# Optimization experiments

Hardware: AMD Instinct MI355X
Metric: run time of the kernel (lower is better)

## Reference

```python
import jax, jax.numpy as jnp
import numpy as np

# Static multi-scale pyramid configuration (matches src_spatial_shapes / level_start_index inputs)
LEVEL_SHAPES = [(128, 128), (64, 64), (32, 32), (16, 16)]  # (H, W) per level
NH, NL, NP = 8, 4, 4  # n_heads, n_levels, n_points
D = 256


def setup_inputs() -> dict:
    key = jax.random.key(0)
    ks = jax.random.split(key, 24)
    N, Lq = 4, 8192
    Lin = sum(h * w for h, w in LEVEL_SHAPES)  # 21760
    d_ff = 4 * D
    inp = {
        "tgt": jax.random.normal(ks[0], (N, Lq, D), jnp.float32),
        "query_pos": jax.random.normal(ks[1], (N, Lq, D), jnp.float32),
        "reference_points": jax.random.uniform(ks[2], (N, Lq, NL, 2), jnp.float32),
        "src": jax.random.normal(ks[3], (N, Lin, D), jnp.float32),
        "src_spatial_shapes": jnp.array(LEVEL_SHAPES, dtype=jnp.int64),
        "level_start_index": jnp.array(np.cumsum([0] + [h * w for h, w in LEVEL_SHAPES[:-1]]), dtype=jnp.int64),
        "src_padding_mask": jnp.zeros((N, Lin), dtype=bool),
        # MSDeformAttn params
        "W_off": jax.random.normal(ks[4], (D, NH * NL * NP * 2), jnp.float32) * 0.01,
        "b_off": jax.random.normal(ks[5], (NH * NL * NP * 2,), jnp.float32) * 0.01,
        "W_attn": jax.random.normal(ks[6], (D, NH * NL * NP), jnp.float32) * 0.02,
        "b_attn": jnp.zeros((NH * NL * NP,), jnp.float32),
        "W_val": jax.random.normal(ks[7], (D, D), jnp.float32) * 0.02,
        "b_val": jnp.zeros((D,), jnp.float32),
        "W_out": jax.random.normal(ks[8], (D, D), jnp.float32) * 0.02,
        "b_out": jnp.zeros((D,), jnp.float32),
        # LN + MLP params
        "ln1_g": jnp.ones((D,), jnp.float32),
        "ln1_b": jnp.zeros((D,), jnp.float32),
        "W_fc1": jax.random.normal(ks[9], (D, d_ff), jnp.float32) * 0.02,
        "b_fc1": jnp.zeros((d_ff,), jnp.float32),
        "W_fc2": jax.random.normal(ks[10], (d_ff, D), jnp.float32) * 0.02,
        "b_fc2": jnp.zeros((D,), jnp.float32),
        "ln2_g": jnp.ones((D,), jnp.float32),
        "ln2_b": jnp.zeros((D,), jnp.float32),
    }
    return inp


def _layer_norm(x, g, b, eps=1e-5):
    x32 = x.astype(jnp.float32)
    m = x32.mean(-1, keepdims=True)
    v = x32.var(-1, keepdims=True)
    return (((x32 - m) * jax.lax.rsqrt(v + eps)) * g + b).astype(x.dtype)


def _sample_level(value_flat, H, W, loc):
    # value_flat: [N, H*W, NH, hd]; loc: [N, Lq, NH, NP, 2] in [0,1]
    # torch.grid_sample align_corners=False, padding_mode='zeros'
    x = loc[..., 0] * W - 0.5
    y = loc[..., 1] * H - 0.5
    x0 = jnp.floor(x)
    y0 = jnp.floor(y)
    dx, dy = x - x0, y - y0
    N, Lq, nh, P = x.shape
    hd = value_flat.shape[-1]
    corners = [
        (x0, y0, (1.0 - dx) * (1.0 - dy)),
        (x0 + 1.0, y0, dx * (1.0 - dy)),
        (x0, y0 + 1.0, (1.0 - dx) * dy),
        (x0 + 1.0, y0 + 1.0, dx * dy),
    ]
    out = jnp.zeros((N, Lq * P, nh, hd), value_flat.dtype)
    for cx, cy, w in corners:
        valid = (cx >= 0) & (cx <= W - 1) & (cy >= 0) & (cy <= H - 1)
        ix = jnp.clip(cx, 0, W - 1).astype(jnp.int32)
        iy = jnp.clip(cy, 0, H - 1).astype(jnp.int32)
        idx = (iy * W + ix).transpose(0, 1, 3, 2).reshape(N, Lq * P, nh)[..., None]
        v = jnp.take_along_axis(value_flat, idx, axis=1)  # [N, Lq*P, NH, hd]
        ww = (w * valid).transpose(0, 1, 3, 2).reshape(N, Lq * P, nh)[..., None]
        out = out + v * ww
    return out.reshape(N, Lq, P, nh, hd)  # [N, Lq, NP, NH, hd]


def reference(tgt, query_pos, reference_points, src, src_spatial_shapes,
              level_start_index, src_padding_mask,
              W_off, b_off, W_attn, b_attn, W_val, b_val, W_out, b_out,
              ln1_g, ln1_b, W_fc1, b_fc1, W_fc2, b_fc2, ln2_g, ln2_b):
    N, Lq, _ = tgt.shape
    hd = D // NH
    q = tgt + query_pos

    # value projection + padding mask
    value = src @ W_val + b_val
    value = jnp.where(src_padding_mask[..., None], 0.0, value)
    value = value.reshape(N, -1, NH, hd)

    # sampling offsets and attention weights
    off = (q @ W_off + b_off).reshape(N, Lq, NH, NL, NP, 2)
    aw = (q @ W_attn + b_attn).reshape(N, Lq, NH, NL * NP)
    aw = jax.nn.softmax(aw, axis=-1).reshape(N, Lq, NH, NL, NP)

    # normalize offsets by (W, H) per level
    normalizer = jnp.array([[w, h] for (h, w) in LEVEL_SHAPES], jnp.float32)  # [NL, 2]
    loc = reference_points[:, :, None, :, None, :] + off / normalizer[None, None, None, :, None, :]

    out = jnp.zeros((N, Lq, NH, hd), value.dtype)
    start = 0
    for l, (H, W) in enumerate(LEVEL_SHAPES):
        vflat = value[:, start:start + H * W]
        start += H * W
        sampled = _sample_level(vflat, H, W, loc[:, :, :, l])  # [N, Lq, NP, NH, hd]
        w_l = aw[:, :, :, l].transpose(0, 1, 3, 2)[..., None]  # [N, Lq, NP, NH, 1]
        out = out + (sampled * w_l).sum(axis=2)
    attn_out = out.reshape(N, Lq, D) @ W_out + b_out

    # residual + LN + MLP (named 'gelu' but is ReLU in source) + LN
    x = _layer_norm(tgt + attn_out, ln1_g, ln1_b)
    h = jax.nn.relu(x @ W_fc1 + b_fc1) @ W_fc2 + b_fc2
    x = _layer_norm(x + h, ln2_g, ln2_b)
    return x
```

## Files before the change

### kernel.cpp

```cpp
#include <hip/hip_runtime.h>
#include <hip/hip_bf16.h>

constexpr int NB    = 4;
constexpr int LQ    = 8192;
constexpr int DM    = 256;
constexpr int NHEAD = 8;
constexpr int HD    = 32;
constexpr int LIN   = 21760;
constexpr int DFF   = 1024;
constexpr int MQ    = NB * LQ;
constexpr int MV    = NB * LIN;

typedef __attribute__((ext_vector_type(8))) short short8;
typedef __attribute__((ext_vector_type(4))) float f32x4;

__device__ __forceinline__ ushort f2b(float f) {
  union { __hip_bfloat16 h; ushort u; } c;
  c.h = __float2bfloat16(f);
  return c.u;
}
__device__ __forceinline__ float b2f(ushort u) {
  return __uint_as_float((unsigned int)u << 16);
}

__device__ __forceinline__ void load_lds16(const ushort* g, ushort* l) {
  __builtin_amdgcn_global_load_lds(
      (const __attribute__((address_space(1))) void*)g,
      (__attribute__((address_space(3))) void*)l, 16, 0, 0);
}

__global__ __launch_bounds__(256) void k_packw(const float* __restrict__ W,
                                               ushort* __restrict__ P,
                                               int K, int Nsrc, int n_base) {
  __shared__ float T[32][33];
  const int k0 = blockIdx.x * 32, n0 = blockIdx.y * 32;
  const int t = threadIdx.x;
  {
    const int r = t >> 3, c4 = t & 7;
    const float4 v = *reinterpret_cast<const float4*>(
        &W[(size_t)(k0 + r) * Nsrc + n0 + c4 * 4]);
    T[r][c4 * 4 + 0] = v.x;
    T[r][c4 * 4 + 1] = v.y;
    T[r][c4 * 4 + 2] = v.z;
    T[r][c4 * 4 + 3] = v.w;
  }
  __syncthreads();
  const int dn = t >> 3, q = t & 7;
  const int n = n_base + n0 + dn;
  const int k = k0 + q * 4;
  const int Tt = n >> 4, fr = n & 15, kg = (k >> 3) & 3;
  const int idx = Tt * (K >> 5) + (k >> 5);
  ushort4 o;
  o.x = f2b(T[q * 4 + 0][dn]);
  o.y = f2b(T[q * 4 + 1][dn]);
  o.z = f2b(T[q * 4 + 2][dn]);
  o.w = f2b(T[q * 4 + 3][dn]);
  *reinterpret_cast<ushort4*>(&P[(size_t)idx * 512 + (kg * 16 + fr) * 8 + (k & 7)]) = o;
}

template<int MODE, int ASRC>
__global__ __launch_bounds__(256) void k_gemm(
    const void* __restrict__ Ap, const float* __restrict__ A2,
    const ushort* __restrict__ BP,
    const float* __restrict__ bias, const float* __restrict__ bias2,
    void* __restrict__ out0, void* __restrict__ out1,
    int M, int N, int K) {
  __shared__ __align__(16) ushort SMEM[17408];
  ushort* As = SMEM;
  const int m0 = blockIdx.x * 128, n0 = blockIdx.y * 128;
  const int t = threadIdx.x, w = t >> 6, l = t & 63;
  const int wr = (w >> 1) * 64, wc = (w & 1) * 64;
  const int fr = l & 15, kg = l >> 4;
  const int lrow = l >> 3;
  const int sg = (l & 7) ^ lrow;
  const int Kg = K >> 5;

  f32x4 acc[4][4];
#pragma unroll
  for (int i = 0; i < 4; ++i)
#pragma unroll
    for (int j = 0; j < 4; ++j) acc[i][j] = f32x4{0.f, 0.f, 0.f, 0.f};

  const float* Af = (const float*)Ap;

  for (int k0 = 0; k0 < K; k0 += 64) {
    float4 fa[4][2];
#pragma unroll
    for (int i = 0; i < 4; ++i) {
      const float* ap = Af + (size_t)(m0 + i * 32 + w * 8 + lrow) * K + k0 + sg * 8;
      fa[i][0] = *reinterpret_cast<const float4*>(ap);
      fa[i][1] = *reinterpret_cast<const float4*>(ap + 4);
      if constexpr (ASRC == 2) {
        const float* ap2 = A2 + (size_t)(m0 + i * 32 + w * 8 + lrow) * K + k0 + sg * 8;
        const float4 x = *reinterpret_cast<const float4*>(ap2);
        const float4 y = *reinterpret_cast<const float4*>(ap2 + 4);
        fa[i][0].x += x.x; fa[i][0].y += x.y; fa[i][0].z += x.z; fa[i][0].w += x.w;
        fa[i][1].x += y.x; fa[i][1].y += y.y; fa[i][1].z += y.z; fa[i][1].w += y.w;
      }
    }
    __syncthreads();
#pragma unroll
    for (int i = 0; i < 4; ++i) {
      uint4 u;
      u.x = (unsigned int)f2b(fa[i][0].x) | ((unsigned int)f2b(fa[i][0].y) << 16);
      u.y = (unsigned int)f2b(fa[i][0].z) | ((unsigned int)f2b(fa[i][0].w) << 16);
      u.z = (unsigned int)f2b(fa[i][1].x) | ((unsigned int)f2b(fa[i][1].y) << 16);
      u.w = (unsigned int)f2b(fa[i][1].z) | ((unsigned int)f2b(fa[i][1].w) << 16);
      *reinterpret_cast<uint4*>(As + i * 2048 + w * 512 + l * 8) = u;
    }
    __syncthreads();
#pragma unroll
    for (int kk = 0; kk < 2; ++kk) {
      short8 a[4], b[4];
#pragma unroll
      for (int i = 0; i < 4; ++i)
        a[i] = *reinterpret_cast<const short8*>(
            &As[(wr + i * 16 + fr) * 64 + ((kk * 4 + kg) ^ (fr & 7)) * 8]);
#pragma unroll
      for (int i = 0; i < 4; ++i)
        b[i] = *reinterpret_cast<const short8*>(
            BP + ((size_t)((n0 >> 4) + (w & 1) * 4 + i) * Kg + (k0 >> 5) + kk) * 512 + l * 8);
#pragma unroll
      for (int mi = 0; mi < 4; ++mi)
#pragma unroll
        for (int ni = 0; ni < 4; ++ni)
          acc[mi][ni] = __builtin_amdgcn_mfma_f32_16x16x32_bf16(
              b[ni], a[mi], acc[mi][ni], 0, 0, 0);
    }
  }

  if constexpr (MODE == 0) {
    ushort (*LC)[136] = (ushort(*)[136])SMEM;
    __syncthreads();
#pragma unroll
    for (int ni = 0; ni < 4; ++ni) {
      const float4 bv = *reinterpret_cast<const float4*>(&bias[n0 + wc + ni * 16 + kg * 4]);
#pragma unroll
      for (int mi = 0; mi < 4; ++mi) {
        ushort4 p;
        p.x = f2b(acc[mi][ni][0] + bv.x);
        p.y = f2b(acc[mi][ni][1] + bv.y);
        p.z = f2b(acc[mi][ni][2] + bv.z);
        p.w = f2b(acc[mi][ni][3] + bv.w);
        *reinterpret_cast<ushort4*>(&LC[wr + mi * 16 + fr][wc + ni * 16 + kg * 4]) = p;
      }
    }
    __syncthreads();
    const int c = t & 15, rb = t >> 4;
#pragma unroll
    for (int i = 0; i < 8; ++i) {
      const int r = rb + i * 16;
      const uint4 vv = *reinterpret_cast<const uint4*>(&LC[r][c * 8]);
      *reinterpret_cast<uint4*>((ushort*)out0 + (size_t)(m0 + r) * N + n0 + c * 8) = vv;
    }
  } else {
    float (*LF)[132] = (float(*)[132])SMEM;
    const float* bp = (n0 < 256) ? bias + n0 : bias2;
    float* op = (n0 < 256) ? (float*)out0 + n0 : (float*)out1;
    const int ostride = (n0 < 256) ? 256 : 128;
#pragma unroll
    for (int p = 0; p < 2; ++p) {
      __syncthreads();
      if ((w >> 1) == p) {
#pragma unroll
        for (int ni = 0; ni < 4; ++ni) {
          const float4 bv = *reinterpret_cast<const float4*>(&bp[wc + ni * 16 + kg * 4]);
#pragma unroll
          for (int mi = 0; mi < 4; ++mi) {
            float4 v;
            v.x = acc[mi][ni][0] + bv.x; v.y = acc[mi][ni][1] + bv.y;
            v.z = acc[mi][ni][2] + bv.z; v.w = acc[mi][ni][3] + bv.w;
            *reinterpret_cast<float4*>(&LF[mi * 16 + fr][wc + ni * 16 + kg * 4]) = v;
          }
        }
      }
      __syncthreads();
      const int c = t & 31, rb = t >> 5;
#pragma unroll
      for (int i = 0; i < 8; ++i) {
        const int r = rb + i * 8;
        const float4 vv = *reinterpret_cast<const float4*>(&LF[r][c * 4]);
        *reinterpret_cast<float4*>(&op[(size_t)(m0 + p * 64 + r) * ostride + c * 4]) = vv;
      }
    }
  }
}

__global__ __launch_bounds__(256) void k_outln(
    const ushort* __restrict__ A, const ushort* __restrict__ BP,
    const float* __restrict__ bias, const float* __restrict__ res,
    const float* __restrict__ g, const float* __restrict__ bvec,
    ushort* __restrict__ out, int K) {
  __shared__ __align__(16) ushort SMEM[17408];
  ushort* As = SMEM;
  const int m0 = blockIdx.x * 64;
  const int t = threadIdx.x, w = t >> 6, l = t & 63;
  const int wc = w * 64;
  const int fr = l & 15, kg = l >> 4;
  const int lrow = l >> 3;
  const int sg = (l & 7) ^ lrow;
  const int Kg = K >> 5;

  f32x4 acc[4][4];
#pragma unroll
  for (int i = 0; i < 4; ++i)
#pragma unroll
    for (int j = 0; j < 4; ++j) acc[i][j] = f32x4{0.f, 0.f, 0.f, 0.f};

  for (int k0 = 0; k0 < K; k0 += 64) {
    __syncthreads();
#pragma unroll
    for (int i = 0; i < 2; ++i)
      load_lds16(A + (size_t)(m0 + i * 32 + w * 8 + lrow) * K + k0 + sg * 8,
                 As + i * 2048 + w * 512);
    __syncthreads();
#pragma unroll
    for (int kk = 0; kk < 2; ++kk) {
      short8 a[4], b[4];
#pragma unroll
      for (int i = 0; i < 4; ++i)
        a[i] = *reinterpret_cast<const short8*>(
            &As[(i * 16 + fr) * 64 + ((kk * 4 + kg) ^ (fr & 7)) * 8]);
#pragma unroll
      for (int i = 0; i < 4; ++i)
        b[i] = *reinterpret_cast<const short8*>(
            BP + ((size_t)(w * 4 + i) * Kg + (k0 >> 5) + kk) * 512 + l * 8);
#pragma unroll
      for (int mi = 0; mi < 4; ++mi)
#pragma unroll
        for (int ni = 0; ni < 4; ++ni)
          acc[mi][ni] = __builtin_amdgcn_mfma_f32_16x16x32_bf16(
              b[ni], a[mi], acc[mi][ni], 0, 0, 0);
    }
  }

  ushort (*LY)[272] = (ushort(*)[272])SMEM;
  __syncthreads();
#pragma unroll
  for (int ni = 0; ni < 4; ++ni) {
    const float4 bv = *reinterpret_cast<const float4*>(&bias[wc + ni * 16 + kg * 4]);
#pragma unroll
    for (int mi = 0; mi < 4; ++mi) {
      ushort4 p;
      p.x = f2b(acc[mi][ni][0] + bv.x);
      p.y = f2b(acc[mi][ni][1] + bv.y);
      p.z = f2b(acc[mi][ni][2] + bv.z);
      p.w = f2b(acc[mi][ni][3] + bv.w);
      *reinterpret_cast<ushort4*>(&LY[mi * 16 + fr][wc + ni * 16 + kg * 4]) = p;
    }
  }
  __syncthreads();

  const int c = t & 31, rb = t >> 5;
#pragma unroll
  for (int i = 0; i < 8; ++i) {
    const int r = rb + i * 8;
    const uint4 yy = *reinterpret_cast<const uint4*>(&LY[r][c * 8]);
    const unsigned int yw[4] = {yy.x, yy.y, yy.z, yy.w};
    float v[8];
#pragma unroll
    for (int j = 0; j < 4; ++j) {
      v[2 * j]     = __uint_as_float(yw[j] << 16);
      v[2 * j + 1] = __uint_as_float(yw[j] & 0xffff0000u);
    }
    const float* rp = res + (size_t)(m0 + r) * 256 + c * 8;
    const float4 r0 = *reinterpret_cast<const float4*>(rp);
    const float4 r1 = *reinterpret_cast<const float4*>(rp + 4);
    v[0] += r0.x; v[1] += r0.y; v[2] += r0.z; v[3] += r0.w;
    v[4] += r1.x; v[5] += r1.y; v[6] += r1.z; v[7] += r1.w;
    float s = 0.f, ss = 0.f;
#pragma unroll
    for (int j = 0; j < 8; ++j) { s += v[j]; ss += v[j] * v[j]; }
#pragma unroll
    for (int o = 1; o < 32; o <<= 1) {
      s  += __shfl_xor(s, o);
      ss += __shfl_xor(ss, o);
    }
    const float m = s * (1.f / 256.f);
    const float inv = rsqrtf(ss * (1.f / 256.f) - m * m + 1e-5f);
    const float4 g0 = *reinterpret_cast<const float4*>(&g[c * 8]);
    const float4 g1 = *reinterpret_cast<const float4*>(&g[c * 8 + 4]);
    const float4 b0 = *reinterpret_cast<const float4*>(&bvec[c * 8]);
    const float4 b1 = *reinterpret_cast<const float4*>(&bvec[c * 8 + 4]);
    uint4 u;
    u.x = (unsigned int)f2b((v[0] - m) * inv * g0.x + b0.x) |
          ((unsigned int)f2b((v[1] - m) * inv * g0.y + b0.y) << 16);
    u.y = (unsigned int)f2b((v[2] - m) * inv * g0.z + b0.z) |
          ((unsigned int)f2b((v[3] - m) * inv * g0.w + b0.w) << 16);
    u.z = (unsigned int)f2b((v[4] - m) * inv * g1.x + b1.x) |
          ((unsigned int)f2b((v[5] - m) * inv * g1.y + b1.y) << 16);
    u.w = (unsigned int)f2b((v[6] - m) * inv * g1.z + b1.z) |
          ((unsigned int)f2b((v[7] - m) * inv * g1.w + b1.w) << 16);
    *reinterpret_cast<uint4*>(out + (size_t)(m0 + r) * 256 + c * 8) = u;
  }
}

__global__ __launch_bounds__(256) void k_ffn(
    const ushort* __restrict__ X, const ushort* __restrict__ W1P,
    const float* __restrict__ bb1, const ushort* __restrict__ W2P,
    const float* __restrict__ bb2, const float* __restrict__ g2,
    const float* __restrict__ b2v, float* __restrict__ out) {
  __shared__ __align__(16) ushort SMEM[24576];
  ushort* Xs = SMEM;
  ushort* Hs = SMEM + 16384;
  const int m0 = blockIdx.x * 64;
  const int t = threadIdx.x, w = t >> 6, l = t & 63;
  const int fr = l & 15, kg = l >> 4;

#pragma unroll
  for (int i = 0; i < 8; ++i) {
    const int gi = w * 8 + i;
    const int row = gi * 2 + (l >> 5);
    load_lds16(X + (size_t)(m0 + row) * 256 + (((l & 31) ^ (row & 7)) * 8),
               Xs + gi * 512);
  }
  __syncthreads();

  f32x4 acc2[4][4];
#pragma unroll
  for (int i = 0; i < 4; ++i)
#pragma unroll
    for (int j = 0; j < 4; ++j) acc2[i][j] = f32x4{0.f, 0.f, 0.f, 0.f};

  for (int c = 0; c < 8; ++c) {
    f32x4 acc1[4][2];
#pragma unroll
    for (int i = 0; i < 4; ++i)
#pragma unroll
      for (int j = 0; j < 2; ++j) acc1[i][j] = f32x4{0.f, 0.f, 0.f, 0.f};
#pragma unroll
    for (int ks = 0; ks < 8; ++ks) {
      short8 a[4], b[2];
#pragma unroll
      for (int mi = 0; mi < 4; ++mi)
        a[mi] = *reinterpret_cast<const short8*>(
            &Xs[(mi * 16 + fr) * 256 + ((ks * 4 + kg) ^ (fr & 7)) * 8]);
#pragma unroll
      for (int ni = 0; ni < 2; ++ni)
        b[ni] = *reinterpret_cast<const short8*>(
            W1P + ((size_t)(c * 8 + w * 2 + ni) * 8 + ks) * 512 + l * 8);
#pragma unroll
      for (int mi = 0; mi < 4; ++mi)
#pragma unroll
        for (int ni = 0; ni < 2; ++ni)
          acc1[mi][ni] = __builtin_amdgcn_mfma_f32_16x16x32_bf16(
              b[ni], a[mi], acc1[mi][ni], 0, 0, 0);
    }
    __syncthreads();
#pragma unroll
    for (int ni = 0; ni < 2; ++ni) {
      const float4 bv = *reinterpret_cast<const float4*>(
          &bb1[c * 128 + w * 32 + ni * 16 + kg * 4]);
#pragma unroll
      for (int mi = 0; mi < 4; ++mi) {
        const int row = mi * 16 + fr;
        const int gcol = w * 4 + ni * 2 + (kg >> 1);
        ushort4 p;
        p.x = f2b(fmaxf(acc1[mi][ni][0] + bv.x, 0.f));
        p.y = f2b(fmaxf(acc1[mi][ni][1] + bv.y, 0.f));
        p.z = f2b(fmaxf(acc1[mi][ni][2] + bv.z, 0.f));
        p.w = f2b(fmaxf(acc1[mi][ni][3] + bv.w, 0.f));
        *reinterpret_cast<ushort4*>(
            &Hs[row * 128 + ((gcol ^ (fr & 7)) * 8) + (kg & 1) * 4]) = p;
      }
    }
    __syncthreads();
#pragma unroll
    for (int ks2 = 0; ks2 < 4; ++ks2) {
      short8 a2[4], b2[4];
#pragma unroll
      for (int mi = 0; mi < 4; ++mi)
        a2[mi] = *reinterpret_cast<const short8*>(
            &Hs[(mi * 16 + fr) * 128 + ((ks2 * 4 + kg) ^ (fr & 7)) * 8]);
#pragma unroll
      for (int ni = 0; ni < 4; ++ni)
        b2[ni] = *reinterpret_cast<const short8*>(
            W2P + ((size_t)(w * 4 + ni) * 32 + c * 4 + ks2) * 512 + l * 8);
#pragma unroll
      for (int mi = 0; mi < 4; ++mi)
#pragma unroll
        for (int ni = 0; ni < 4; ++ni)
          acc2[mi][ni] = __builtin_amdgcn_mfma_f32_16x16x32_bf16(
              b2[ni], a2[mi], acc2[mi][ni], 0, 0, 0);
    }
  }

#pragma unroll
  for (int ni = 0; ni < 4; ++ni) {
    const int colb = w * 64 + ni * 16 + kg * 4;
    const float4 bv = *reinterpret_cast<const float4*>(&bb2[colb]);
    const int g = w * 8 + ni * 2 + (kg >> 1);
#pragma unroll
    for (int mi = 0; mi < 4; ++mi) {
      const int row = mi * 16 + fr;
      const ushort4 xr = *reinterpret_cast<const ushort4*>(
          &Xs[row * 256 + ((g ^ (fr & 7)) * 8) + (kg & 1) * 4]);
      acc2[mi][ni][0] += bv.x + b2f(xr.x);
      acc2[mi][ni][1] += bv.y + b2f(xr.y);
      acc2[mi][ni][2] += bv.z + b2f(xr.z);
      acc2[mi][ni][3] += bv.w + b2f(xr.w);
    }
  }
  __syncthreads();

  ushort (*LY)[272] = (ushort(*)[272])SMEM;
#pragma unroll
  for (int ni = 0; ni < 4; ++ni) {
#pragma unroll
    for (int mi = 0; mi < 4; ++mi) {
      ushort4 p;
      p.x = f2b(acc2[mi][ni][0]);
      p.y = f2b(acc2[mi][ni][1]);
      p.z = f2b(acc2[mi][ni][2]);
      p.w = f2b(acc2[mi][ni][3]);
      *reinterpret_cast<ushort4*>(&LY[mi * 16 + fr][w * 64 + ni * 16 + kg * 4]) = p;
    }
  }
  __syncthreads();

  const int cc = t & 31, rb = t >> 5;
#pragma unroll
  for (int i = 0; i < 8; ++i) {
    const int r = rb + i * 8;
    const uint4 yy = *reinterpret_cast<const uint4*>(&LY[r][cc * 8]);
    const unsigned int yw[4] = {yy.x, yy.y, yy.z, yy.w};
    float v[8];
#pragma unroll
    for (int j = 0; j < 4; ++j) {
      v[2 * j]     = __uint_as_float(yw[j] << 16);
      v[2 * j + 1] = __uint_as_float(yw[j] & 0xffff0000u);
    }
    float s = 0.f, ss = 0.f;
#pragma unroll
    for (int j = 0; j < 8; ++j) { s += v[j]; ss += v[j] * v[j]; }
#pragma unroll
    for (int o = 1; o < 32; o <<= 1) {
      s  += __shfl_xor(s, o);
      ss += __shfl_xor(ss, o);
    }
    const float m = s * (1.f / 256.f);
    const float inv = rsqrtf(ss * (1.f / 256.f) - m * m + 1e-5f);
    const float4 g0 = *reinterpret_cast<const float4*>(&g2[cc * 8]);
    const float4 g1 = *reinterpret_cast<const float4*>(&g2[cc * 8 + 4]);
    const float4 b0 = *reinterpret_cast<const float4*>(&b2v[cc * 8]);
    const float4 b1 = *reinterpret_cast<const float4*>(&b2v[cc * 8 + 4]);
    float* opp = out + (size_t)(m0 + r) * 256 + cc * 8;
    float4 q0, q1;
    q0.x = (v[0] - m) * inv * g0.x + b0.x;
    q0.y = (v[1] - m) * inv * g0.y + b0.y;
    q0.z = (v[2] - m) * inv * g0.z + b0.z;
    q0.w = (v[3] - m) * inv * g0.w + b0.w;
    q1.x = (v[4] - m) * inv * g1.x + b1.x;
    q1.y = (v[5] - m) * inv * g1.y + b1.y;
    q1.z = (v[6] - m) * inv * g1.z + b1.z;
    q1.w = (v[7] - m) * inv * g1.w + b1.w;
    *reinterpret_cast<float4*>(opp) = q0;
    *reinterpret_cast<float4*>(opp + 4) = q1;
  }
}

__global__ __launch_bounds__(256) void k_softmax(const float* __restrict__ logits,
                                                 float* __restrict__ aw) {
  const int g = blockIdx.x * 256 + threadIdx.x;
  const float* p = logits + (size_t)g * 16;
  float mx = p[0];
#pragma unroll
  for (int i = 1; i < 16; ++i) mx = fmaxf(mx, p[i]);
  float e[16], s = 0.f;
#pragma unroll
  for (int i = 0; i < 16; ++i) { e[i] = __expf(p[i] - mx); s += e[i]; }
  const float inv = 1.f / s;
  float* o = aw + (size_t)g * 16;
#pragma unroll
  for (int i = 0; i < 16; ++i) o[i] = e[i] * inv;
}

__global__ __launch_bounds__(256) void k_sample(
    const float* __restrict__ refp, const float* __restrict__ off_ws,
    const float* __restrict__ aw_ws, const ushort* __restrict__ value,
    ushort* __restrict__ pre) {
  const int tid = blockIdx.x * 256 + threadIdx.x;
  const int cg = tid & 3;
  const int h  = (tid >> 2) & 7;
  const int nq = tid >> 5;
  const int n  = nq >> 13;

  const float* rp = refp + (size_t)nq * 8;
  const float* op = off_ws + (size_t)nq * DM + h * 32;
  const float* ap = aw_ws + (size_t)nq * 128 + h * 16;
  const ushort* vb = value + (size_t)n * LIN * DM + h * HD + cg * 8;

  float acc[8];
#pragma unroll
  for (int j = 0; j < 8; ++j) acc[j] = 0.f;

  const int WL[4] = {128, 64, 32, 16};
  const int ST[4] = {0, 16384, 20480, 21504};

#pragma unroll
  for (int lvl = 0; lvl < 4; ++lvl) {
    const int Wl = WL[lvl];
    const float fW = (float)Wl;
    const float invW = 1.f / fW;
    const float rx = rp[lvl * 2 + 0];
    const float ry = rp[lvl * 2 + 1];
    const ushort* vl = vb + (size_t)ST[lvl] * DM;
#pragma unroll
    for (int p = 0; p < 4; ++p) {
      const float xx = (rx + op[(lvl * 4 + p) * 2 + 0] * invW) * fW - 0.5f;
      const float yy = (ry + op[(lvl * 4 + p) * 2 + 1] * invW) * fW - 0.5f;
      const float a = ap[lvl * 4 + p];
      const float x0 = floorf(xx), y0 = floorf(yy);
      const float dx = xx - x0, dy = yy - y0;
      const bool vx0 = (x0 >= 0.f) && (x0 <= fW - 1.f);
      const bool vx1 = (x0 + 1.f >= 0.f) && (x0 + 1.f <= fW - 1.f);
      const bool vy0 = (y0 >= 0.f) && (y0 <= fW - 1.f);
      const bool vy1 = (y0 + 1.f >= 0.f) && (y0 + 1.f <= fW - 1.f);
      const int ix0 = min(max((int)x0, 0), Wl - 1);
      const int ix1 = min(max((int)x0 + 1, 0), Wl - 1);
      const int iy0 = min(max((int)y0, 0), Wl - 1);
      const int iy1 = min(max((int)y0 + 1, 0), Wl - 1);
      const float w00 = (vx0 && vy0) ? (1.f - dx) * (1.f - dy) * a : 0.f;
      const float w10 = (vx1 && vy0) ? dx * (1.f - dy) * a : 0.f;
      const float w01 = (vx0 && vy1) ? (1.f - dx) * dy * a : 0.f;
      const float w11 = (vx1 && vy1) ? dx * dy * a : 0.f;
      const ushort* r0 = vl + (size_t)iy0 * Wl * DM;
      const ushort* r1 = vl + (size_t)iy1 * Wl * DM;
      const uint4 u00 = *reinterpret_cast<const uint4*>(r0 + ix0 * DM);
      const uint4 u10 = *reinterpret_cast<const uint4*>(r0 + ix1 * DM);
      const uint4 u01 = *reinterpret_cast<const uint4*>(r1 + ix0 * DM);
      const uint4 u11 = *reinterpret_cast<const uint4*>(r1 + ix1 * DM);
      const unsigned int uu00[4] = {u00.x, u00.y, u00.z, u00.w};
      const unsigned int uu10[4] = {u10.x, u10.y, u10.z, u10.w};
      const unsigned int uu01[4] = {u01.x, u01.y, u01.z, u01.w};
      const unsigned int uu11[4] = {u11.x, u11.y, u11.z, u11.w};
#pragma unroll
      for (int i = 0; i < 4; ++i) {
        acc[2 * i]     += __uint_as_float(uu00[i] << 16) * w00;
        acc[2 * i + 1] += __uint_as_float(uu00[i] & 0xffff0000u) * w00;
        acc[2 * i]     += __uint_as_float(uu10[i] << 16) * w10;
        acc[2 * i + 1] += __uint_as_float(uu10[i] & 0xffff0000u) * w10;
        acc[2 * i]     += __uint_as_float(uu01[i] << 16) * w01;
        acc[2 * i + 1] += __uint_as_float(uu01[i] & 0xffff0000u) * w01;
        acc[2 * i]     += __uint_as_float(uu11[i] << 16) * w11;
        acc[2 * i + 1] += __uint_as_float(uu11[i] & 0xffff0000u) * w11;
      }
    }
  }

  uint4 o;
  o.x = (unsigned int)f2b(acc[0]) | ((unsigned int)f2b(acc[1]) << 16);
  o.y = (unsigned int)f2b(acc[2]) | ((unsigned int)f2b(acc[3]) << 16);
  o.z = (unsigned int)f2b(acc[4]) | ((unsigned int)f2b(acc[5]) << 16);
  o.w = (unsigned int)f2b(acc[6]) | ((unsigned int)f2b(acc[7]) << 16);
  *reinterpret_cast<uint4*>(pre + (size_t)nq * DM + h * HD + cg * 8) = o;
}

extern "C" void kernel_launch(void* const* d_in, const int* in_sizes, int n_in,
                              void* d_out, int out_size, void* d_ws, size_t ws_size,
                              hipStream_t stream) {
  const float* tgt   = (const float*)d_in[0];
  const float* qpos  = (const float*)d_in[1];
  const float* refp  = (const float*)d_in[2];
  const float* src   = (const float*)d_in[3];
  const float* Woff  = (const float*)d_in[7];
  const float* boff  = (const float*)d_in[8];
  const float* Wattn = (const float*)d_in[9];
  const float* battn = (const float*)d_in[10];
  const float* Wval  = (const float*)d_in[11];
  const float* bval  = (const float*)d_in[12];
  const float* Wout  = (const float*)d_in[13];
  const float* bout  = (const float*)d_in[14];
  const float* g1    = (const float*)d_in[15];
  const float* b1    = (const float*)d_in[16];
  const float* W1    = (const float*)d_in[17];
  const float* bb1   = (const float*)d_in[18];
  const float* W2    = (const float*)d_in[19];
  const float* bb2   = (const float*)d_in[20];
  const float* g2    = (const float*)d_in[21];
  const float* b2v   = (const float*)d_in[22];
  float* out = (float*)d_out;

  char* ws = (char*)d_ws;
  float*  offb   = (float*)(ws + 0);
  ushort* valueb = (ushort*)(ws + 44564480);
  ushort* preb   = (ushort*)(ws + 89128960);
  float*  logits = (float*)(ws + 105906176);
  float*  awb    = (float*)(ws + 122683392);
  ushort* xb     = (ushort*)(ws + 0);
  ushort* wvalP  = (ushort*)(ws + 156237824);
  ushort* wqP    = wvalP + 65536;
  ushort* woutP  = wqP + 98304;
  ushort* w1P    = woutP + 65536;
  ushort* w2P    = w1P + 262144;

  hipLaunchKernelGGL(k_packw, dim3(8, 8), dim3(256), 0, stream, Wval, wvalP, 256, 256, 0);
  hipLaunchKernelGGL(k_packw, dim3(8, 8), dim3(256), 0, stream, Woff, wqP, 256, 256, 0);
  hipLaunchKernelGGL(k_packw, dim3(8, 4), dim3(256), 0, stream, Wattn, wqP, 256, 128, 256);
  hipLaunchKernelGGL(k_packw, dim3(8, 8), dim3(256), 0, stream, Wout, woutP, 256, 256, 0);
  hipLaunchKernelGGL(k_packw, dim3(8, 32), dim3(256), 0, stream, W1, w1P, 256, 1024, 0);
  hipLaunchKernelGGL(k_packw, dim3(32, 8), dim3(256), 0, stream, W2, w2P, 1024, 256, 0);

  hipLaunchKernelGGL((k_gemm<0, 1>), dim3(MV / 128, 2), dim3(256), 0, stream,
                     (const void*)src, (const float*)nullptr, wvalP, bval,
                     (const float*)nullptr, (void*)valueb, (void*)nullptr,
                     MV, DM, DM);

  hipLaunchKernelGGL((k_gemm<3, 2>), dim3(MQ / 128, 3), dim3(256), 0, stream,
                     (const void*)tgt, qpos, wqP, boff, battn,
                     (void*)offb, (void*)logits, MQ, 384, DM);

  hipLaunchKernelGGL(k_softmax, dim3(MQ * 8 / 256), dim3(256), 0, stream, logits, awb);

  hipLaunchKernelGGL(k_sample, dim3(MQ * NHEAD * 4 / 256), dim3(256), 0, stream,
                     refp, offb, awb, valueb, preb);

  hipLaunchKernelGGL(k_outln, dim3(MQ / 64), dim3(256), 0, stream,
                     preb, woutP, bout, tgt, g1, b1, xb, DM);

  hipLaunchKernelGGL(k_ffn, dim3(MQ / 64), dim3(256), 0, stream,
                     xb, w1P, bb1, w2P, bb2, g2, b2v, out);
}
```

Measured before the change: 260.9 us.

## Fuse softmax into logit GEMM, store offsets as bf16, merge weight packing

Splits the query projection into a bf16 offset GEMM and a separate logit GEMM whose epilogue computes the per-head softmax, which removes the standalone softmax kernel and its fp32 logits round trip. The sampling offsets are now written and read as bf16, which halves that traffic but lowers offset precision. The sampler gains vectorized loads and a swizzled block order for cache locality, and the six weight-pack launches become one kernel. The tgt+qpos input is now read twice, once by each of the two query GEMMs.

```diff
diff --git a/kernel.cpp b/kernel.cpp
--- a/kernel.cpp
+++ b/kernel.cpp
@@ -29,11 +29,25 @@
       (__attribute__((address_space(3))) void*)l, 16, 0, 0);
 }
 
-__global__ __launch_bounds__(256) void k_packw(const float* __restrict__ W,
-                                               ushort* __restrict__ P,
-                                               int K, int Nsrc, int n_base) {
+__global__ __launch_bounds__(256) void k_packall(
+    const float* __restrict__ Wval, const float* __restrict__ Woff,
+    const float* __restrict__ Wattn, const float* __restrict__ Wout,
+    const float* __restrict__ W1, const float* __restrict__ W2,
+    ushort* __restrict__ wvalP, ushort* __restrict__ wqP,
+    ushort* __restrict__ woutP, ushort* __restrict__ w1P,
+    ushort* __restrict__ w2P) {
+  const int bid = blockIdx.x;
+  const float* W; ushort* P; int K, Nsrc, n_base, local;
+  if (bid < 64)       { W = Wval;  P = wvalP; K = 256;  Nsrc = 256;  n_base = 0;   local = bid; }
+  else if (bid < 128) { W = Woff;  P = wqP;   K = 256;  Nsrc = 256;  n_base = 0;   local = bid - 64; }
+  else if (bid < 160) { W = Wattn; P = wqP;   K = 256;  Nsrc = 128;  n_base = 256; local = bid - 128; }
+  else if (bid < 224) { W = Wout;  P = woutP; K = 256;  Nsrc = 256;  n_base = 0;   local = bid - 160; }
+  else if (bid < 480) { W = W1;    P = w1P;   K = 256;  Nsrc = 1024; n_base = 0;   local = bid - 224; }
+  else                { W = W2;    P = w2P;   K = 1024; Nsrc = 256;  n_base = 0;   local = bid - 480; }
+  const int kb = local % (K >> 5), nb = local / (K >> 5);
+  const int k0 = kb * 32, n0 = nb * 32;
+
   __shared__ float T[32][33];
-  const int k0 = blockIdx.x * 32, n0 = blockIdx.y * 32;
   const int t = threadIdx.x;
   {
     const int r = t >> 3, c4 = t & 7;
@@ -62,9 +76,8 @@
 __global__ __launch_bounds__(256) void k_gemm(
     const void* __restrict__ Ap, const float* __restrict__ A2,
     const ushort* __restrict__ BP,
-    const float* __restrict__ bias, const float* __restrict__ bias2,
-    void* __restrict__ out0, void* __restrict__ out1,
-    int M, int N, int K) {
+    const float* __restrict__ bias,
+    void* __restrict__ out0, int M, int N, int K) {
   __shared__ __align__(16) ushort SMEM[17408];
   ushort* As = SMEM;
   const int m0 = blockIdx.x * 128, n0 = blockIdx.y * 128;
@@ -129,59 +142,143 @@
     }
   }
 
-  if constexpr (MODE == 0) {
-    ushort (*LC)[136] = (ushort(*)[136])SMEM;
-    __syncthreads();
-#pragma unroll
-    for (int ni = 0; ni < 4; ++ni) {
-      const float4 bv = *reinterpret_cast<const float4*>(&bias[n0 + wc + ni * 16 + kg * 4]);
-#pragma unroll
-      for (int mi = 0; mi < 4; ++mi) {
-        ushort4 p;
-        p.x = f2b(acc[mi][ni][0] + bv.x);
-        p.y = f2b(acc[mi][ni][1] + bv.y);
-        p.z = f2b(acc[mi][ni][2] + bv.z);
-        p.w = f2b(acc[mi][ni][3] + bv.w);
-        *reinterpret_cast<ushort4*>(&LC[wr + mi * 16 + fr][wc + ni * 16 + kg * 4]) = p;
-      }
-    }
-    __syncthreads();
-    const int c = t & 15, rb = t >> 4;
-#pragma unroll
-    for (int i = 0; i < 8; ++i) {
-      const int r = rb + i * 16;
-      const uint4 vv = *reinterpret_cast<const uint4*>(&LC[r][c * 8]);
-      *reinterpret_cast<uint4*>((ushort*)out0 + (size_t)(m0 + r) * N + n0 + c * 8) = vv;
-    }
-  } else {
-    float (*LF)[132] = (float(*)[132])SMEM;
-    const float* bp = (n0 < 256) ? bias + n0 : bias2;
-    float* op = (n0 < 256) ? (float*)out0 + n0 : (float*)out1;
-    const int ostride = (n0 < 256) ? 256 : 128;
-#pragma unroll
-    for (int p = 0; p < 2; ++p) {
-      __syncthreads();
-      if ((w >> 1) == p) {
-#pragma unroll
-        for (int ni = 0; ni < 4; ++ni) {
-          const float4 bv = *reinterpret_cast<const float4*>(&bp[wc + ni * 16 + kg * 4]);
-#pragma unroll
-          for (int mi = 0; mi < 4; ++mi) {
-            float4 v;
-            v.x = acc[mi][ni][0] + bv.x; v.y = acc[mi][ni][1] + bv.y;
-            v.z = acc[mi][ni][2] + bv.z; v.w = acc[mi][ni][3] + bv.w;
-            *reinterpret_cast<float4*>(&LF[mi * 16 + fr][wc + ni * 16 + kg * 4]) = v;
-          }
+  ushort (*LC)[136] = (ushort(*)[136])SMEM;
+  __syncthreads();
+#pragma unroll
+  for (int ni = 0; ni < 4; ++ni) {
+    const float4 bv = *reinterpret_cast<const float4*>(&bias[n0 + wc + ni * 16 + kg * 4]);
+#pragma unroll
+    for (int mi = 0; mi < 4; ++mi) {
+      ushort4 p;
+      p.x = f2b(acc[mi][ni][0] + bv.x);
+      p.y = f2b(acc[mi][ni][1] + bv.y);
+      p.z = f2b(acc[mi][ni][2] + bv.z);
+      p.w = f2b(acc[mi][ni][3] + bv.w);
+      *reinterpret_cast<ushort4*>(&LC[wr + mi * 16 + fr][wc + ni * 16 + kg * 4]) = p;
+    }
+  }
+  __syncthreads();
+  const int c = t & 15, rb = t >> 4;
+#pragma unroll
+  for (int i = 0; i < 8; ++i) {
+    const int r = rb + i * 16;
+    const uint4 vv = *reinterpret_cast<const uint4*>(&LC[r][c * 8]);
+    *reinterpret_cast<uint4*>((ushort*)out0 + (size_t)(m0 + r) * N + n0 + c * 8) = vv;
+  }
+}
+
+__global__ __launch_bounds__(256) void k_qlogit(
+    const float* __restrict__ tgt, const float* __restrict__ qpos,
+    const ushort* __restrict__ BP, const float* __restrict__ battn,
+    float* __restrict__ awb) {
+  __shared__ __align__(16) ushort SMEM[17408];
+  ushort* As = SMEM;
+  const int m0 = blockIdx.x * 128;
+  const int t = threadIdx.x, w = t >> 6, l = t & 63;
+  const int wc = (w & 1) * 64;
+  const int fr = l & 15, kg = l >> 4;
+  const int lrow = l >> 3;
+  const int sg = (l & 7) ^ lrow;
+
+  f32x4 acc[4][4];
+#pragma unroll
+  for (int i = 0; i < 4; ++i)
+#pragma unroll
+    for (int j = 0; j < 4; ++j) acc[i][j] = f32x4{0.f, 0.f, 0.f, 0.f};
+
+  for (int k0 = 0; k0 < 256; k0 += 64) {
+    float4 fa[4][2];
+#pragma unroll
+    for (int i = 0; i < 4; ++i) {
+      const float* ap = tgt + (size_t)(m0 + i * 32 + w * 8 + lrow) * 256 + k0 + sg * 8;
+      const float* ap2 = qpos + (size_t)(m0 + i * 32 + w * 8 + lrow) * 256 + k0 + sg * 8;
+      fa[i][0] = *reinterpret_cast<const float4*>(ap);
+      fa[i][1] = *reinterpret_cast<const float4*>(ap + 4);
+      const float4 x = *reinterpret_cast<const float4*>(ap2);
+      const float4 y = *reinterpret_cast<const float4*>(ap2 + 4);
+      fa[i][0].x += x.x; fa[i][0].y += x.y; fa[i][0].z += x.z; fa[i][0].w += x.w;
+      fa[i][1].x += y.x; fa[i][1].y += y.y; fa[i][1].z += y.z; fa[i][1].w += y.w;
+    }
+    __syncthreads();
+#pragma unroll
+    for (int i = 0; i < 4; ++i) {
+      uint4 u;
+      u.x = (unsigned int)f2b(fa[i][0].x) | ((unsigned int)f2b(fa[i][0].y) << 16);
+      u.y = (unsigned int)f2b(fa[i][0].z) | ((unsigned int)f2b(fa[i][0].w) << 16);
+      u.z = (unsigned int)f2b(fa[i][1].x) | ((unsigned int)f2b(fa[i][1].y) << 16);
+      u.w = (unsigned int)f2b(fa[i][1].z) | ((unsigned int)f2b(fa[i][1].w) << 16);
+      *reinterpret_cast<uint4*>(As + i * 2048 + w * 512 + l * 8) = u;
+    }
+    __syncthreads();
+#pragma unroll
+    for (int kk = 0; kk < 2; ++kk) {
+      short8 a[4], b[4];
+#pragma unroll
+      for (int i = 0; i < 4; ++i)
+        a[i] = *reinterpret_cast<const short8*>(
+            &As[((w >> 1) * 64 + i * 16 + fr) * 64 + ((kk * 4 + kg) ^ (fr & 7)) * 8]);
+#pragma unroll
+      for (int i = 0; i < 4; ++i)
+        b[i] = *reinterpret_cast<const short8*>(
+            BP + ((size_t)(16 + (w & 1) * 4 + i) * 8 + (k0 >> 5) + kk) * 512 + l * 8);
+#pragma unroll
+      for (int mi = 0; mi < 4; ++mi)
+#pragma unroll
+        for (int ni = 0; ni < 4; ++ni)
+          acc[mi][ni] = __builtin_amdgcn_mfma_f32_16x16x32_bf16(
+              b[ni], a[mi], acc[mi][ni], 0, 0, 0);
+    }
+  }
+
+  float (*LF)[132] = (float(*)[132])SMEM;
+#pragma unroll
+  for (int p = 0; p < 2; ++p) {
+    __syncthreads();
+    if ((w >> 1) == p) {
+#pragma unroll
+      for (int ni = 0; ni < 4; ++ni) {
+        const float4 bv = *reinterpret_cast<const float4*>(&battn[wc + ni * 16 + kg * 4]);
+#pragma unroll
+        for (int mi = 0; mi < 4; ++mi) {
+          float4 v;
+          v.x = acc[mi][ni][0] + bv.x; v.y = acc[mi][ni][1] + bv.y;
+          v.z = acc[mi][ni][2] + bv.z; v.w = acc[mi][ni][3] + bv.w;
+          *reinterpret_cast<float4*>(&LF[mi * 16 + fr][wc + ni * 16 + kg * 4]) = v;
         }
       }
-      __syncthreads();
-      const int c = t & 31, rb = t >> 5;
-#pragma unroll
-      for (int i = 0; i < 8; ++i) {
-        const int r = rb + i * 8;
-        const float4 vv = *reinterpret_cast<const float4*>(&LF[r][c * 4]);
-        *reinterpret_cast<float4*>(&op[(size_t)(m0 + p * 64 + r) * ostride + c * 4]) = vv;
-      }
+    }
+    __syncthreads();
+#pragma unroll
+    for (int gi = 0; gi < 2; ++gi) {
+      const int g = t + gi * 256;
+      const int row = g >> 3, hh = g & 7;
+      const float* src = &LF[row][hh * 16];
+      float e[16];
+      float4 v0 = *reinterpret_cast<const float4*>(src);
+      float4 v1 = *reinterpret_cast<const float4*>(src + 4);
+      float4 v2 = *reinterpret_cast<const float4*>(src + 8);
+      float4 v3 = *reinterpret_cast<const float4*>(src + 12);
+      e[0]=v0.x; e[1]=v0.y; e[2]=v0.z; e[3]=v0.w;
+      e[4]=v1.x; e[5]=v1.y; e[6]=v1.z; e[7]=v1.w;
+      e[8]=v2.x; e[9]=v2.y; e[10]=v2.z; e[11]=v2.w;
+      e[12]=v3.x; e[13]=v3.y; e[14]=v3.z; e[15]=v3.w;
+      float mx = e[0];
+#pragma unroll
+      for (int i = 1; i < 16; ++i) mx = fmaxf(mx, e[i]);
+      float s = 0.f;
+#pragma unroll
+      for (int i = 0; i < 16; ++i) { e[i] = __expf(e[i] - mx); s += e[i]; }
+      const float inv = 1.f / s;
+      float* o = awb + (size_t)(m0 + p * 64 + row) * 128 + hh * 16;
+      float4 q;
+      q.x = e[0]*inv; q.y = e[1]*inv; q.z = e[2]*inv; q.w = e[3]*inv;
+      *reinterpret_cast<float4*>(o) = q;
+      q.x = e[4]*inv; q.y = e[5]*inv; q.z = e[6]*inv; q.w = e[7]*inv;
+      *reinterpret_cast<float4*>(o + 4) = q;
+      q.x = e[8]*inv; q.y = e[9]*inv; q.z = e[10]*inv; q.w = e[11]*inv;
+      *reinterpret_cast<float4*>(o + 8) = q;
+      q.x = e[12]*inv; q.y = e[13]*inv; q.z = e[14]*inv; q.w = e[15]*inv;
+      *reinterpret_cast<float4*>(o + 12) = q;
     }
   }
 }
@@ -459,35 +556,23 @@
   }
 }
 
-__global__ __launch_bounds__(256) void k_softmax(const float* __restrict__ logits,
-                                                 float* __restrict__ aw) {
-  const int g = blockIdx.x * 256 + threadIdx.x;
-  const float* p = logits + (size_t)g * 16;
-  float mx = p[0];
-#pragma unroll
-  for (int i = 1; i < 16; ++i) mx = fmaxf(mx, p[i]);
-  float e[16], s = 0.f;
-#pragma unroll
-  for (int i = 0; i < 16; ++i) { e[i] = __expf(p[i] - mx); s += e[i]; }
-  const float inv = 1.f / s;
-  float* o = aw + (size_t)g * 16;
-#pragma unroll
-  for (int i = 0; i < 16; ++i) o[i] = e[i] * inv;
-}
-
 __global__ __launch_bounds__(256) void k_sample(
-    const float* __restrict__ refp, const float* __restrict__ off_ws,
-    const float* __restrict__ aw_ws, const ushort* __restrict__ value,
+    const float* __restrict__ refp, const ushort* __restrict__ offb,
+    const float* __restrict__ awb, const ushort* __restrict__ value,
     ushort* __restrict__ pre) {
-  const int tid = blockIdx.x * 256 + threadIdx.x;
+  const int bid = ((blockIdx.x & 7) << 9) | (blockIdx.x >> 3);
+  const int tid = bid * 256 + threadIdx.x;
   const int cg = tid & 3;
   const int h  = (tid >> 2) & 7;
   const int nq = tid >> 5;
   const int n  = nq >> 13;
 
-  const float* rp = refp + (size_t)nq * 8;
-  const float* op = off_ws + (size_t)nq * DM + h * 32;
-  const float* ap = aw_ws + (size_t)nq * 128 + h * 16;
+  const float4 r01 = *reinterpret_cast<const float4*>(refp + (size_t)nq * 8);
+  const float4 r23 = *reinterpret_cast<const float4*>(refp + (size_t)nq * 8 + 4);
+  const float rxs[4] = {r01.x, r01.z, r23.x, r23.z};
+  const float rys[4] = {r01.y, r01.w, r23.y, r23.w};
+  const ushort* op = offb + (size_t)nq * 256 + h * 32;
+  const float*  ap = awb + (size_t)nq * 128 + h * 16;
   const ushort* vb = value + (size_t)n * LIN * DM + h * HD + cg * 8;
 
   float acc[8];
@@ -502,14 +587,19 @@
     const int Wl = WL[lvl];
     const float fW = (float)Wl;
     const float invW = 1.f / fW;
-    const float rx = rp[lvl * 2 + 0];
-    const float ry = rp[lvl * 2 + 1];
+    const float rx = rxs[lvl], ry = rys[lvl];
     const ushort* vl = vb + (size_t)ST[lvl] * DM;
+    const uint4 ov = *reinterpret_cast<const uint4*>(op + lvl * 8);
+    const float4 a4 = *reinterpret_cast<const float4*>(ap + lvl * 4);
+    const unsigned int ow[4] = {ov.x, ov.y, ov.z, ov.w};
+    const float aa[4] = {a4.x, a4.y, a4.z, a4.w};
 #pragma unroll
     for (int p = 0; p < 4; ++p) {
-      const float xx = (rx + op[(lvl * 4 + p) * 2 + 0] * invW) * fW - 0.5f;
-      const float yy = (ry + op[(lvl * 4 + p) * 2 + 1] * invW) * fW - 0.5f;
-      const float a = ap[lvl * 4 + p];
+      const float ox = __uint_as_float(ow[p] << 16);
+      const float oy = __uint_as_float(ow[p] & 0xffff0000u);
+      const float xx = (rx + ox * invW) * fW - 0.5f;
+      const float yy = (ry + oy * invW) * fW - 0.5f;
+      const float a = aa[p];
       const float x0 = floorf(xx), y0 = floorf(yy);
       const float dx = xx - x0, dy = yy - y0;
       const bool vx0 = (x0 >= 0.f) && (x0 <= fW - 1.f);
@@ -582,11 +672,10 @@
   float* out = (float*)d_out;
 
   char* ws = (char*)d_ws;
-  float*  offb   = (float*)(ws + 0);
+  ushort* offb   = (ushort*)(ws + 0);
   ushort* valueb = (ushort*)(ws + 44564480);
   ushort* preb   = (ushort*)(ws + 89128960);
-  float*  logits = (float*)(ws + 105906176);
-  float*  awb    = (float*)(ws + 122683392);
+  float*  awb    = (float*)(ws + 105906176);
   ushort* xb     = (ushort*)(ws + 0);
   ushort* wvalP  = (ushort*)(ws + 156237824);
   ushort* wqP    = wvalP + 65536;
@@ -594,23 +683,20 @@
   ushort* w1P    = woutP + 65536;
   ushort* w2P    = w1P + 262144;
 
-  hipLaunchKernelGGL(k_packw, dim3(8, 8), dim3(256), 0, stream, Wval, wvalP, 256, 256, 0);
-  hipLaunchKernelGGL(k_packw, dim3(8, 8), dim3(256), 0, stream, Woff, wqP, 256, 256, 0);
-  hipLaunchKernelGGL(k_packw, dim3(8, 4), dim3(256), 0, stream, Wattn, wqP, 256, 128, 256);
-  hipLaunchKernelGGL(k_packw, dim3(8, 8), dim3(256), 0, stream, Wout, woutP, 256, 256, 0);
-  hipLaunchKernelGGL(k_packw, dim3(8, 32), dim3(256), 0, stream, W1, w1P, 256, 1024, 0);
-  hipLaunchKernelGGL(k_packw, dim3(32, 8), dim3(256), 0, stream, W2, w2P, 1024, 256, 0);
+  hipLaunchKernelGGL(k_packall, dim3(736), dim3(256), 0, stream,
+                     Wval, Woff, Wattn, Wout, W1, W2,
+                     wvalP, wqP, woutP, w1P, w2P);
 
   hipLaunchKernelGGL((k_gemm<0, 1>), dim3(MV / 128, 2), dim3(256), 0, stream,
                      (const void*)src, (const float*)nullptr, wvalP, bval,
-                     (const float*)nullptr, (void*)valueb, (void*)nullptr,
-                     MV, DM, DM);
-
-  hipLaunchKernelGGL((k_gemm<3, 2>), dim3(MQ / 128, 3), dim3(256), 0, stream,
-                     (const void*)tgt, qpos, wqP, boff, battn,
-                     (void*)offb, (void*)logits, MQ, 384, DM);
-
-  hipLaunchKernelGGL(k_softmax, dim3(MQ * 8 / 256), dim3(256), 0, stream, logits, awb);
+                     (void*)valueb, MV, DM, DM);
+
+  hipLaunchKernelGGL((k_gemm<0, 2>), dim3(MQ / 128, 2), dim3(256), 0, stream,
+                     (const void*)tgt, qpos, wqP, boff,
+                     (void*)offb, MQ, DM, DM);
+
+  hipLaunchKernelGGL(k_qlogit, dim3(MQ / 128), dim3(256), 0, stream,
+                     tgt, qpos, wqP, battn, awb);
 
   hipLaunchKernelGGL(k_sample, dim3(MQ * NHEAD * 4 / 256), dim3(256), 0, stream,
                      refp, offb, awb, valueb, preb);
```

Result: faster. 219.9 us (-15.7%).
